# Kernel optimization log

Hardware: AMD Instinct MI355X
Metric: run time of the kernel (lower is better)

## Reference

```python
import jax, jax.numpy as jnp
import numpy as np

NUM_RBF = 16
RBF_D_MIN, RBF_D_MAX = 2.0, 22.0
CB_A, CB_B, CB_C = -0.58273431, 0.56802827, -0.54067466
TOP_K = 32
MAX_REL = 32
NPOS = 16
HID = 128
LN_EPS = 1e-5


def _gather_nodes(nodes, idx):
    # nodes: (B, L, D), idx: (B, L, K) -> (B, L, K, D)
    return jax.vmap(lambda n, i: n[i])(nodes, idx)


def _rbf_encode(D):
    mu = jnp.linspace(RBF_D_MIN, RBF_D_MAX, NUM_RBF, dtype=D.dtype)
    sigma = (RBF_D_MAX - RBF_D_MIN) / NUM_RBF
    return jnp.exp(-((D[..., None] - mu) ** 2) / (sigma ** 2))


def setup_inputs() -> dict:
    key = jax.random.key(0)
    ks = jax.random.split(key, 4)
    B, L = 2, 2048
    X = jax.random.normal(ks[0], (B, L, 4, 3), jnp.float32) * 10.0
    residue_mask = jnp.ones((B, L), jnp.float32)
    R_idx = jnp.arange(B * L, dtype=jnp.int32).reshape(B, L)
    chain_labels = jnp.zeros((B, L), jnp.int32)
    # learned params
    W_pos = jax.random.normal(ks[1], (NPOS, 2 * MAX_REL + 2), jnp.float32) * 0.05
    b_pos = jnp.zeros((NPOS,), jnp.float32)
    W_edge = jax.random.normal(ks[2], (HID, 25 * NUM_RBF + NPOS), jnp.float32) * 0.02
    ln_gamma = jnp.ones((HID,), jnp.float32)
    ln_beta = jnp.zeros((HID,), jnp.float32)
    return {"X": X, "residue_mask": residue_mask, "R_idx": R_idx,
            "chain_labels": chain_labels, "W_pos": W_pos, "b_pos": b_pos,
            "W_edge": W_edge, "ln_gamma": ln_gamma, "ln_beta": ln_beta}


def reference(X, residue_mask, R_idx, chain_labels, W_pos, b_pos, W_edge, ln_gamma, ln_beta):
    B, L = X.shape[0], X.shape[1]
    K = min(TOP_K, L)
    # virtual CB from backbone N, CA, C
    N, CA, C = X[..., 0, :], X[..., 1, :], X[..., 2, :]
    b = CA - N
    c = C - CA
    a = jnp.cross(b, c, axis=-1)
    CB = (CB_A * a + CB_B * b + CB_C * c + CA)[..., None, :]
    atoms_5 = jnp.concatenate([X, CB], axis=-2)  # (B, L, 5, 3)
    # kNN on CA coords with invalid residues pushed far away
    diff = CA[:, :, None, :] - CA[:, None, :, :]
    dist_sq = jnp.sum(diff * diff, axis=-1)  # (B, L, L)
    inv_mask = 1.0 - residue_mask
    dist_sq = dist_sq + inv_mask[:, None, :] * 1e6
    _, E_idx = jax.lax.top_k(-dist_sq, K)  # smallest-k indices, (B, L, K)
    # gather neighbor 5-atom coords and compute 25 pairwise distances
    Xf = atoms_5.reshape(B, L, 15)
    Xg = _gather_nodes(Xf, E_idx).reshape(B, L, K, 5, 3)
    d2 = jnp.sum((atoms_5[:, :, None, :, None, :] - Xg[:, :, :, None, :, :]) ** 2, axis=-1)
    D = jnp.sqrt(d2 + 1e-6)  # (B, L, K, 5, 5)
    rbf = _rbf_encode(D).reshape(B, L, K, 25 * NUM_RBF)
    # positional encodings (standard ProteinMPNN form)
    Rg = _gather_nodes(R_idx[..., None], E_idx)[..., 0]  # (B, L, K)
    Cg = _gather_nodes(chain_labels[..., None], E_idx)[..., 0]
    d_rel = Rg - R_idx[:, :, None]
    same_chain = (Cg == chain_labels[:, :, None])
    d_clip = jnp.clip(d_rel + MAX_REL, 0, 2 * MAX_REL)
    d_final = jnp.where(same_chain, d_clip, 2 * MAX_REL + 1)
    oh = jax.nn.one_hot(d_final, 2 * MAX_REL + 2, dtype=rbf.dtype)
    pos_enc = jnp.einsum('blkc,pc->blkp', oh, W_pos) + b_pos
    # edge embedding + layernorm
    edge_input = jnp.concatenate([pos_enc, rbf], axis=-1)  # (B, L, K, 416)
    h = jnp.einsum('blkf,hf->blkh', edge_input, W_edge)
    mean = jnp.mean(h, axis=-1, keepdims=True)
    var = jnp.var(h, axis=-1, keepdims=True)
    E = (h - mean) * jax.lax.rsqrt(var + LN_EPS) * ln_gamma + ln_beta
    return E_idx, E
```

## Files before the change

kernel.cpp:

```cpp
#include <hip/hip_runtime.h>
#include <hip/hip_bf16.h>

#define LEN   2048
#define KNB   32
#define HID   128
#define FS    512

typedef unsigned long long ull;
typedef unsigned int uint32;
typedef float f32x4 __attribute__((ext_vector_type(4)));
typedef __bf16 bf16x8v __attribute__((ext_vector_type(8)));

__device__ __forceinline__ void bar_lgkm() {
    asm volatile("s_waitcnt lgkmcnt(0)" ::: "memory");
    __builtin_amdgcn_s_barrier();
    asm volatile("" ::: "memory");
}

__global__ __launch_bounds__(256) void prep_kernel(
    const float* __restrict__ X, const float* __restrict__ mask,
    const float* __restrict__ W_edge,
    float4* __restrict__ CAm, int* __restrict__ Wf8) {
    const int t = blockIdx.x * 256 + threadIdx.x;
    if (t < 2 * LEN) {
        const float* p = X + (size_t)t * 12;
        CAm[t] = make_float4(p[3], p[4], p[5],
                             __fmul_rn(__fsub_rn(1.0f, mask[t]), 1000000.0f));
    }
    if (t < 13312) {
        const float4 w = ((const float4*)W_edge)[t];
        int r = __builtin_amdgcn_cvt_pk_fp8_f32(w.x, w.y, 0, false);
        r = __builtin_amdgcn_cvt_pk_fp8_f32(w.z, w.w, r, true);
        Wf8[t] = r;
    }
}

__global__ __launch_bounds__(256) void topk_kernel(
    const float4* __restrict__ CAm, float* __restrict__ eidx_out) {
    const int row = blockIdx.x;
    const int b = row >> 11;
    const int i = row & (LEN - 1);
    const int tid = threadIdx.x;

    __shared__ int hist[512];
    __shared__ ull cand[LEN];
    __shared__ int candcnt;
    __shared__ int selB;

    const float4* C = CAm + (size_t)b * LEN;
    const float4 ci = C[i];

    uint32 d2b[8];
#pragma unroll
    for (int q = 0; q < 8; ++q) {
        const float4 cj = C[q * 256 + tid];
        float dx = __fsub_rn(ci.x, cj.x);
        float dy = __fsub_rn(ci.y, cj.y);
        float dz = __fsub_rn(ci.z, cj.z);
        float d2 = __fadd_rn(__fadd_rn(__fmul_rn(dx, dx), __fmul_rn(dy, dy)),
                             __fmul_rn(dz, dz));
        d2 = __fadd_rn(d2, cj.w);
        d2b[q] = __float_as_uint(d2);
    }

    hist[tid] = 0; hist[tid + 256] = 0;
    if (tid == 0) candcnt = 0;
    __syncthreads();
#pragma unroll
    for (int q = 0; q < 8; ++q) atomicAdd(&hist[d2b[q] >> 22], 1);
    __syncthreads();

    if (tid < 64) {
        int loc[8];
        int s = 0;
#pragma unroll
        for (int t = 0; t < 8; ++t) { loc[t] = hist[tid * 8 + t]; s += loc[t]; }
        int incl = s;
#pragma unroll
        for (int off = 1; off < 64; off <<= 1) {
            int o = __shfl_up(incl, off, 64);
            if (tid >= off) incl += o;
        }
        const int excl = incl - s;
        if (excl < KNB && incl >= KNB) {
            int c = excl;
#pragma unroll
            for (int t = 0; t < 8; ++t) {
                int c2 = c + loc[t];
                if (c < KNB && c2 >= KNB) selB = tid * 8 + t;
                c = c2;
            }
        }
    }
    __syncthreads();
    const uint32 B = (uint32)selB;

#pragma unroll
    for (int q = 0; q < 8; ++q) {
        if ((d2b[q] >> 22) <= B) {
            int p = atomicAdd(&candcnt, 1);
            cand[p] = (((ull)d2b[q]) << 32) | (uint32)(q * 256 + tid);
        }
    }
    __syncthreads();
    const int M = candcnt;

    for (int c = tid; c < M; c += 256) {
        const ull k = cand[c];
        int r = 0;
        for (int m = 0; m < M; ++m) r += (cand[m] < k);
        if (r < KNB)
            eidx_out[(size_t)row * KNB + r] = (float)(uint32)(k & 0xFFFFFFFFull);
    }
}

__device__ __forceinline__ void load_res_atoms(const float* __restrict__ p, float* dst) {
    const float Nx = p[0], Ny = p[1], Nz = p[2];
    const float Ax = p[3], Ay = p[4], Az = p[5];
    const float Cx = p[6], Cy = p[7], Cz = p[8];
    const float Ox = p[9], Oy = p[10], Oz = p[11];
    const float bx = Ax - Nx, by = Ay - Ny, bz = Az - Nz;
    const float cx = Cx - Ax, cy = Cy - Ay, cz = Cz - Az;
    const float axv = by * cz - bz * cy;
    const float ayv = bz * cx - bx * cz;
    const float azv = bx * cy - by * cx;
    dst[0] = Nx;  dst[1] = Ny;  dst[2] = Nz;
    dst[3] = Ax;  dst[4] = Ay;  dst[5] = Az;
    dst[6] = Cx;  dst[7] = Cy;  dst[8] = Cz;
    dst[9] = Ox;  dst[10] = Oy; dst[11] = Oz;
    dst[12] = -0.58273431f * axv + 0.56802827f * bx + -0.54067466f * cx + Ax;
    dst[13] = -0.58273431f * ayv + 0.56802827f * by + -0.54067466f * cy + Ay;
    dst[14] = -0.58273431f * azv + 0.56802827f * bz + -0.54067466f * cz + Az;
}

__device__ __forceinline__ int pk4(float a, float b, float c, float d) {
    int r = __builtin_amdgcn_cvt_pk_fp8_f32(a, b, 0, false);
    return __builtin_amdgcn_cvt_pk_fp8_f32(c, d, r, true);
}

#define E1  3.2053337e-1f
#define E3  3.2931300e-2f
#define E5  3.3834001e-3f
#define E7  3.4760500e-4f

__device__ __forceinline__ void compute_features(
    int tid, int Ri, int Ci,
    const float* __restrict__ wposL,
    const int* jR, const int* jC,
    const float (*natoms)[15], const float* iatoms,
    unsigned char* featF8) {
    {
        const int e = tid >> 4, p = tid & 15;
        const int drel = jR[e] - Ri;
        const int same = (jC[e] == Ci);
        int dc = drel + 32;
        dc = dc < 0 ? 0 : (dc > 64 ? 64 : dc);
        const int df = same ? dc : 65;
        const float v = wposL[p * 66 + df];
        const int pb = __builtin_amdgcn_cvt_pk_fp8_f32(v, 0.0f, 0, false);
        featF8[e * FS + ((e & 7) << 4) + p] = (unsigned char)(pb & 0xFF);
    }
#pragma unroll
    for (int it = 0; it < 2; ++it) {
        const int task = tid + it * 512;
        if (task < 800) {
            const int mn = task >> 5, e = task & 31;
            const int m = mn / 5, n = mn - m * 5;
            const float ax = iatoms[m * 3 + 0];
            const float ay = iatoms[m * 3 + 1];
            const float az = iatoms[m * 3 + 2];
            const float* na = &natoms[e][n * 3];
            const float dx = ax - na[0], dy = ay - na[1], dz = az - na[2];
            const float D = sqrtf(dx * dx + dy * dy + dz * dz + 1e-6f);
            const float Dc = fminf(D, 40.0f);
            const float v4 = Dc - 7.3333333f;
            const float A4  = __expf(-0.64f * v4 * v4);
            const float C4  = __expf(1.7066667f * v4);
            const float Ci4 = 1.0f / C4;
            int4 w4;
            {
                const float f3 = A4 * Ci4 * E1;
                const float f2 = f3 * Ci4 * E3;
                const float f1 = f2 * Ci4 * E5;
                const float f0 = f1 * Ci4 * E7;
                w4.x = pk4(f0, f1, f2, f3);
            }
            {
                const float f5 = A4 * C4 * E1;
                const float f6 = f5 * C4 * E3;
                const float f7 = f6 * C4 * E5;
                w4.y = pk4(A4, f5, f6, f7);
            }
            const float v12 = Dc - 18.0f;
            const float A12  = __expf(-0.64f * v12 * v12);
            const float C12  = C4 * 1.24140e-8f;
            const float Ci12 = Ci4 * 8.05543e7f;
            {
                const float f11 = A12 * Ci12 * E1;
                const float f10 = f11 * Ci12 * E3;
                const float f9  = f10 * Ci12 * E5;
                const float f8  = f9  * Ci12 * E7;
                w4.z = pk4(f8, f9, f10, f11);
            }
            {
                const float f13 = A12 * C12 * E1;
                const float f14 = f13 * C12 * E3;
                const float f15 = f14 * C12 * E5;
                w4.w = pk4(A12, f13, f14, f15);
            }
            *(int4*)(featF8 + e * FS + (((1 + mn) ^ (e & 7)) << 4)) = w4;
        }
    }
}

__device__ __forceinline__ void gemm_row(
    const unsigned char* feat, const long* wreg, int lr, int lg,
    f32x4& acc0, f32x4& acc1) {
    const int sw = lr & 7;
    const int mb = lg >> 1;
    const unsigned char* fb0 = feat + lr * FS + (lg & 1) * 8;
    const unsigned char* fb1 = feat + (16 + lr) * FS + (lg & 1) * 8;
#pragma unroll
    for (int ks = 0; ks < 13; ++ks) {
        const int moff = ((2 * ks + mb) ^ sw) << 4;
        const long a0 = *(const long*)(fb0 + moff);
        const long a1 = *(const long*)(fb1 + moff);
        acc0 = __builtin_amdgcn_mfma_f32_16x16x32_fp8_fp8(a0, wreg[ks], acc0, 0, 0, 0);
        acc1 = __builtin_amdgcn_mfma_f32_16x16x32_fp8_fp8(a1, wreg[ks], acc1, 0, 0, 0);
    }
}

__device__ __forceinline__ void ln_store(
    const __bf16* hb, int row, int tid,
    const float* __restrict__ lng, const float* __restrict__ lnb,
    float* __restrict__ outE) {
    const int g = tid >> 4, l2 = tid & 15;
    const bf16x8v hv = *(const bf16x8v*)(hb + g * 132 + l2 * 8);
    float v[8];
#pragma unroll
    for (int k = 0; k < 8; ++k) v[k] = (float)hv[k];
    float s = 0.f, ssq = 0.f;
#pragma unroll
    for (int k = 0; k < 8; ++k) { s += v[k]; ssq += v[k] * v[k]; }
#pragma unroll
    for (int off = 1; off < 16; off <<= 1) {
        s += __shfl_xor(s, off, 64);
        ssq += __shfl_xor(ssq, off, 64);
    }
    const float mean = s * (1.0f / 128.0f);
    const float rstd = rsqrtf(ssq * (1.0f / 128.0f) - mean * mean + 1e-5f);
    float4* ob = (float4*)(outE + ((size_t)row * KNB + g) * HID + l2 * 8);
    const float4 g0 = *(const float4*)(lng + l2 * 8);
    const float4 g1 = *(const float4*)(lng + l2 * 8 + 4);
    const float4 b0 = *(const float4*)(lnb + l2 * 8);
    const float4 b1 = *(const float4*)(lnb + l2 * 8 + 4);
    float4 o0, o1;
    o0.x = (v[0] - mean) * rstd * g0.x + b0.x;
    o0.y = (v[1] - mean) * rstd * g0.y + b0.y;
    o0.z = (v[2] - mean) * rstd * g0.z + b0.z;
    o0.w = (v[3] - mean) * rstd * g0.w + b0.w;
    o1.x = (v[4] - mean) * rstd * g1.x + b1.x;
    o1.y = (v[5] - mean) * rstd * g1.y + b1.y;
    o1.z = (v[6] - mean) * rstd * g1.z + b1.z;
    o1.w = (v[7] - mean) * rstd * g1.w + b1.w;
    ob[0] = o0;
    ob[1] = o1;
}

__global__ __launch_bounds__(512, 4) void edge_kernel(
    const float* __restrict__ X,
    const int* __restrict__ Ridx, const int* __restrict__ Chain,
    const float* __restrict__ W_pos, const float* __restrict__ b_pos,
    const unsigned char* __restrict__ Wf8,
    const float* __restrict__ lng, const float* __restrict__ lnb,
    const float* __restrict__ eidx_f, float* __restrict__ outE) {
    const int tid = threadIdx.x;
    const int row0 = blockIdx.x * 8;
    const int b = row0 >> 11;
    const int i0 = row0 & (LEN - 1);

    __shared__ __align__(16) unsigned char featF8[2][32 * FS];
    __shared__ __align__(16) __bf16 hbA[32 * 132];
    __shared__ __align__(16) __bf16 hbB[32 * 132];
    __shared__ float natoms[8][32][15];
    __shared__ float iatoms[8][16];
    __shared__ float wposL[16 * 66];
    __shared__ int jR[8][KNB], jC[8][KNB];
    __shared__ int riS[8], ciS[8];

    const float* Xb = X + (size_t)b * LEN * 12;

    const int w = tid >> 6, l = tid & 63, lr = l & 15, lg = l >> 4;
    long wreg[13];
    {
        const unsigned char* wb = Wf8 + (size_t)(w * 16 + lr) * 416 + lg * 8;
#pragma unroll
        for (int ks = 0; ks < 13; ++ks)
            wreg[ks] = *(const long*)(wb + ks * 32);
    }

    for (int t = tid; t < 1056; t += 512)
        wposL[t] = W_pos[t] + b_pos[t / 66];
    if (tid < 256) {
        const int r = tid >> 5, e = tid & 31;
        const int j = (int)eidx_f[(size_t)(row0 + r) * KNB + e];
        jR[r][e] = Ridx[b * LEN + j];
        jC[r][e] = Chain[b * LEN + j];
        load_res_atoms(Xb + j * 12, &natoms[r][e][0]);
    } else if (tid < 264) {
        const int r = tid - 256;
        load_res_atoms(Xb + (size_t)(i0 + r) * 12, &iatoms[r][0]);
    } else if (tid < 272) {
        riS[tid - 264] = Ridx[b * LEN + i0 + (tid - 264)];
    } else if (tid < 280) {
        ciS[tid - 272] = Chain[b * LEN + i0 + (tid - 272)];
    }
    bar_lgkm();

    compute_features(tid, riS[0], ciS[0], wposL, jR[0], jC[0],
                     natoms[0], iatoms[0], featF8[0]);
    compute_features(tid, riS[1], ciS[1], wposL, jR[1], jC[1],
                     natoms[1], iatoms[1], featF8[1]);
    bar_lgkm();

    for (int it = 0; it < 4; ++it) {
        const int ra = row0 + 2 * it, rb = ra + 1;

        f32x4 accA0 = {0.f, 0.f, 0.f, 0.f}, accA1 = accA0;
        f32x4 accB0 = accA0, accB1 = accA0;
        gemm_row(featF8[0], wreg, lr, lg, accA0, accA1);
        gemm_row(featF8[1], wreg, lr, lg, accB0, accB1);
#pragma unroll
        for (int rr = 0; rr < 4; ++rr) {
            const int ch = w * 16 + lr;
            hbA[(lg * 4 + rr) * 132 + ch]      = (__bf16)accA0[rr];
            hbA[(16 + lg * 4 + rr) * 132 + ch] = (__bf16)accA1[rr];
            hbB[(lg * 4 + rr) * 132 + ch]      = (__bf16)accB0[rr];
            hbB[(16 + lg * 4 + rr) * 132 + ch] = (__bf16)accB1[rr];
        }
        bar_lgkm();

        ln_store(hbA, ra, tid, lng, lnb, outE);
        ln_store(hbB, rb, tid, lng, lnb, outE);
        if (it < 3) {
            const int na = 2 * it + 2, nb = 2 * it + 3;
            compute_features(tid, riS[na], ciS[na], wposL, jR[na], jC[na],
                             natoms[na], iatoms[na], featF8[0]);
            compute_features(tid, riS[nb], ciS[nb], wposL, jR[nb], jC[nb],
                             natoms[nb], iatoms[nb], featF8[1]);
        }
        bar_lgkm();
    }
}

extern "C" void kernel_launch(void* const* d_in, const int* in_sizes, int n_in,
                              void* d_out, int out_size, void* d_ws, size_t ws_size,
                              hipStream_t stream) {
    const float* X      = (const float*)d_in[0];
    const float* mask   = (const float*)d_in[1];
    const int*   Ridx   = (const int*)d_in[2];
    const int*   Chain  = (const int*)d_in[3];
    const float* W_pos  = (const float*)d_in[4];
    const float* b_pos  = (const float*)d_in[5];
    const float* W_edge = (const float*)d_in[6];
    const float* lng    = (const float*)d_in[7];
    const float* lnb    = (const float*)d_in[8];

    float* out  = (float*)d_out;
    float* eidx = out;
    float* E    = out + (size_t)2 * LEN * KNB;

    float4* CAm = (float4*)d_ws;
    unsigned char* Wf8 = (unsigned char*)d_ws + 2 * LEN * 16;

    const int nrow = 2 * LEN;
    prep_kernel<<<52, 256, 0, stream>>>(X, mask, W_edge, CAm, (int*)Wf8);
    topk_kernel<<<nrow, 256, 0, stream>>>(CAm, eidx);
    edge_kernel<<<nrow / 8, 512, 0, stream>>>(X, Ridx, Chain, W_pos, b_pos, Wf8,
                                              lng, lnb, eidx, E);
}
```

Baseline: 62.23 us.

## Switch edge GEMM to 32x32 MFMA and fuse layernorm in registers

Replaces the 16x16x32 fp8 MFMA per-row GEMM with 32x32x16 fp8 MFMA, computing the transposed product so each lane holds 16 output channels for one edge. LayerNorm statistics are reduced from the accumulators via a shuffle and a small shared partial-sum buffer, which removes the bf16 staging of the hidden vector through LDS and its rounding. Each wave now handles one row and a 32-channel slice, and holds 26 weight registers instead of 13, which raises register pressure.

New measurement: 59.95 us. 1.04x faster.

```diff
diff --git a/kernel.cpp b/kernel.cpp
--- a/kernel.cpp
+++ b/kernel.cpp
@@ -8,8 +8,8 @@
 
 typedef unsigned long long ull;
 typedef unsigned int uint32;
-typedef float f32x4 __attribute__((ext_vector_type(4)));
-typedef __bf16 bf16x8v __attribute__((ext_vector_type(8)));
+typedef float f32x4  __attribute__((ext_vector_type(4)));
+typedef float f32x16 __attribute__((ext_vector_type(16)));
 
 __device__ __forceinline__ void bar_lgkm() {
     asm volatile("s_waitcnt lgkmcnt(0)" ::: "memory");
@@ -213,60 +213,6 @@
     }
 }
 
-__device__ __forceinline__ void gemm_row(
-    const unsigned char* feat, const long* wreg, int lr, int lg,
-    f32x4& acc0, f32x4& acc1) {
-    const int sw = lr & 7;
-    const int mb = lg >> 1;
-    const unsigned char* fb0 = feat + lr * FS + (lg & 1) * 8;
-    const unsigned char* fb1 = feat + (16 + lr) * FS + (lg & 1) * 8;
-#pragma unroll
-    for (int ks = 0; ks < 13; ++ks) {
-        const int moff = ((2 * ks + mb) ^ sw) << 4;
-        const long a0 = *(const long*)(fb0 + moff);
-        const long a1 = *(const long*)(fb1 + moff);
-        acc0 = __builtin_amdgcn_mfma_f32_16x16x32_fp8_fp8(a0, wreg[ks], acc0, 0, 0, 0);
-        acc1 = __builtin_amdgcn_mfma_f32_16x16x32_fp8_fp8(a1, wreg[ks], acc1, 0, 0, 0);
-    }
-}
-
-__device__ __forceinline__ void ln_store(
-    const __bf16* hb, int row, int tid,
-    const float* __restrict__ lng, const float* __restrict__ lnb,
-    float* __restrict__ outE) {
-    const int g = tid >> 4, l2 = tid & 15;
-    const bf16x8v hv = *(const bf16x8v*)(hb + g * 132 + l2 * 8);
-    float v[8];
-#pragma unroll
-    for (int k = 0; k < 8; ++k) v[k] = (float)hv[k];
-    float s = 0.f, ssq = 0.f;
-#pragma unroll
-    for (int k = 0; k < 8; ++k) { s += v[k]; ssq += v[k] * v[k]; }
-#pragma unroll
-    for (int off = 1; off < 16; off <<= 1) {
-        s += __shfl_xor(s, off, 64);
-        ssq += __shfl_xor(ssq, off, 64);
-    }
-    const float mean = s * (1.0f / 128.0f);
-    const float rstd = rsqrtf(ssq * (1.0f / 128.0f) - mean * mean + 1e-5f);
-    float4* ob = (float4*)(outE + ((size_t)row * KNB + g) * HID + l2 * 8);
-    const float4 g0 = *(const float4*)(lng + l2 * 8);
-    const float4 g1 = *(const float4*)(lng + l2 * 8 + 4);
-    const float4 b0 = *(const float4*)(lnb + l2 * 8);
-    const float4 b1 = *(const float4*)(lnb + l2 * 8 + 4);
-    float4 o0, o1;
-    o0.x = (v[0] - mean) * rstd * g0.x + b0.x;
-    o0.y = (v[1] - mean) * rstd * g0.y + b0.y;
-    o0.z = (v[2] - mean) * rstd * g0.z + b0.z;
-    o0.w = (v[3] - mean) * rstd * g0.w + b0.w;
-    o1.x = (v[4] - mean) * rstd * g1.x + b1.x;
-    o1.y = (v[5] - mean) * rstd * g1.y + b1.y;
-    o1.z = (v[6] - mean) * rstd * g1.z + b1.z;
-    o1.w = (v[7] - mean) * rstd * g1.w + b1.w;
-    ob[0] = o0;
-    ob[1] = o1;
-}
-
 __global__ __launch_bounds__(512, 4) void edge_kernel(
     const float* __restrict__ X,
     const int* __restrict__ Ridx, const int* __restrict__ Chain,
@@ -280,23 +226,26 @@
     const int i0 = row0 & (LEN - 1);
 
     __shared__ __align__(16) unsigned char featF8[2][32 * FS];
-    __shared__ __align__(16) __bf16 hbA[32 * 132];
-    __shared__ __align__(16) __bf16 hbB[32 * 132];
     __shared__ float natoms[8][32][15];
     __shared__ float iatoms[8][16];
     __shared__ float wposL[16 * 66];
+    __shared__ __align__(16) float pS[2][32][4], pQ[2][32][4];
+    __shared__ float gbuf[HID], bbuf[HID];
     __shared__ int jR[8][KNB], jC[8][KNB];
     __shared__ int riS[8], ciS[8];
 
     const float* Xb = X + (size_t)b * LEN * 12;
 
-    const int w = tid >> 6, l = tid & 63, lr = l & 15, lg = l >> 4;
-    long wreg[13];
+    const int w = tid >> 6, l = tid & 63;
+    const int rowsel = w >> 2, cg = w & 3;
+    const int e32 = l & 31, hi = l >> 5;
+
+    long wreg[26];
     {
-        const unsigned char* wb = Wf8 + (size_t)(w * 16 + lr) * 416 + lg * 8;
-#pragma unroll
-        for (int ks = 0; ks < 13; ++ks)
-            wreg[ks] = *(const long*)(wb + ks * 32);
+        const unsigned char* wb = Wf8 + (size_t)(cg * 32 + e32) * 416 + hi * 8;
+#pragma unroll
+        for (int ks = 0; ks < 26; ++ks)
+            wreg[ks] = *(const long*)(wb + ks * 16);
     }
 
     for (int t = tid; t < 1056; t += 512)
@@ -314,6 +263,10 @@
         riS[tid - 264] = Ridx[b * LEN + i0 + (tid - 264)];
     } else if (tid < 280) {
         ciS[tid - 272] = Chain[b * LEN + i0 + (tid - 272)];
+    } else if (tid >= 384) {
+        const int t2 = tid - 384;
+        gbuf[t2] = lng[t2];
+        bbuf[t2] = lnb[t2];
     }
     bar_lgkm();
 
@@ -324,24 +277,53 @@
     bar_lgkm();
 
     for (int it = 0; it < 4; ++it) {
-        const int ra = row0 + 2 * it, rb = ra + 1;
-
-        f32x4 accA0 = {0.f, 0.f, 0.f, 0.f}, accA1 = accA0;
-        f32x4 accB0 = accA0, accB1 = accA0;
-        gemm_row(featF8[0], wreg, lr, lg, accA0, accA1);
-        gemm_row(featF8[1], wreg, lr, lg, accB0, accB1);
-#pragma unroll
-        for (int rr = 0; rr < 4; ++rr) {
-            const int ch = w * 16 + lr;
-            hbA[(lg * 4 + rr) * 132 + ch]      = (__bf16)accA0[rr];
-            hbA[(16 + lg * 4 + rr) * 132 + ch] = (__bf16)accA1[rr];
-            hbB[(lg * 4 + rr) * 132 + ch]      = (__bf16)accB0[rr];
-            hbB[(16 + lg * 4 + rr) * 132 + ch] = (__bf16)accB1[rr];
+        const int myrow = row0 + 2 * it + rowsel;
+
+        f32x16 acc = {0.f, 0.f, 0.f, 0.f, 0.f, 0.f, 0.f, 0.f,
+                      0.f, 0.f, 0.f, 0.f, 0.f, 0.f, 0.f, 0.f};
+        {
+            const unsigned char* fb = featF8[rowsel] + e32 * FS + hi * 8;
+            const int sw = e32 & 7;
+#pragma unroll
+            for (int ks = 0; ks < 26; ++ks) {
+                const long a = *(const long*)(fb + ((ks ^ sw) << 4));
+                acc = __builtin_amdgcn_mfma_f32_32x32x16_fp8_fp8(wreg[ks], a, acc, 0, 0, 0);
+            }
+        }
+        {
+            float s = 0.f, q = 0.f;
+#pragma unroll
+            for (int r = 0; r < 16; ++r) { s += acc[r]; q += acc[r] * acc[r]; }
+            s += __shfl_xor(s, 32, 64);
+            q += __shfl_xor(q, 32, 64);
+            if (hi == 0) {
+                pS[rowsel][e32][cg] = s;
+                pQ[rowsel][e32][cg] = q;
+            }
         }
         bar_lgkm();
 
-        ln_store(hbA, ra, tid, lng, lnb, outE);
-        ln_store(hbB, rb, tid, lng, lnb, outE);
+        {
+            const float4 ps = *(const float4*)&pS[rowsel][e32][0];
+            const float4 pq = *(const float4*)&pQ[rowsel][e32][0];
+            const float s = ps.x + ps.y + ps.z + ps.w;
+            const float q = pq.x + pq.y + pq.z + pq.w;
+            const float mean = s * (1.0f / 128.0f);
+            const float rstd = rsqrtf(q * (1.0f / 128.0f) - mean * mean + 1e-5f);
+            const int cb = cg * 32 + hi * 4;
+            float* orow = outE + ((size_t)myrow * KNB + e32) * HID + cb;
+#pragma unroll
+            for (int j = 0; j < 4; ++j) {
+                const float4 gg = *(const float4*)&gbuf[cb + 8 * j];
+                const float4 bb = *(const float4*)&bbuf[cb + 8 * j];
+                float4 o;
+                o.x = (acc[4 * j + 0] - mean) * rstd * gg.x + bb.x;
+                o.y = (acc[4 * j + 1] - mean) * rstd * gg.y + bb.y;
+                o.z = (acc[4 * j + 2] - mean) * rstd * gg.z + bb.z;
+                o.w = (acc[4 * j + 3] - mean) * rstd * gg.w + bb.w;
+                *(float4*)(orow + 8 * j) = o;
+            }
+        }
         if (it < 3) {
             const int na = 2 * it + 2, nb = 2 * it + 3;
             compute_features(tid, riS[na], ciS[na], wposL, jR[na], jC[na],
```
